# Kernel optimization log

Measured on AMD Instinct MI355X. Metric: run time of the kernel, lower is better.

The kernel has to match this reference:

```python
import jax, jax.numpy as jnp
import numpy as np

N_NODES = 50000
N_EDGES = 800000
VOCAB = 1000
EMBED = 64
HIDDEN = 64
N_CLASSES = 10
N_GRAPHS = 512


def setup_inputs() -> dict:
    key = jax.random.key(0)
    ks = jax.random.split(key, 10)
    tokens = jax.random.randint(ks[0], (N_NODES,), 0, VOCAB)
    edge_index = jax.random.randint(ks[1], (2, N_EDGES), 0, N_NODES)
    batch = jnp.sort(jax.random.randint(ks[2], (N_NODES,), 0, N_GRAPHS))
    emb = jax.random.normal(ks[3], (VOCAB, EMBED), jnp.float32) * 0.02
    emb = emb.at[0].set(0.0)  # padding_idx=0
    W1 = jax.random.normal(ks[4], (EMBED, HIDDEN), jnp.float32) * (1.0 / np.sqrt(EMBED))
    b1 = jnp.zeros((HIDDEN,), jnp.float32)
    W2 = jax.random.normal(ks[5], (HIDDEN, HIDDEN), jnp.float32) * (1.0 / np.sqrt(HIDDEN))
    b2 = jnp.zeros((HIDDEN,), jnp.float32)
    lin_W = jax.random.normal(ks[6], (HIDDEN, N_CLASSES), jnp.float32) * (1.0 / np.sqrt(HIDDEN))
    lin_b = jnp.zeros((N_CLASSES,), jnp.float32)
    return {"tokens": tokens, "edge_index": edge_index, "batch": batch,
            "emb": emb, "W1": W1, "b1": b1, "W2": W2, "b2": b2,
            "lin_W": lin_W, "lin_b": lin_b}


def _gcn_conv(x, src, dst, W, b, n_nodes):
    # PyG GCNConv: add self-loops, symmetric normalization D^-1/2 (A+I) D^-1/2
    ones = jnp.ones((src.shape[0],), x.dtype)
    deg = jax.ops.segment_sum(ones, dst, num_segments=n_nodes) + 1.0  # self-loop
    dis = jnp.where(deg > 0, jax.lax.rsqrt(deg), 0.0)
    h = x @ W  # linear first (no bias)
    coef = dis[src] * dis[dst]                      # [E]
    msg = h[src] * coef[:, None]                    # gather + scale
    agg = jax.ops.segment_sum(msg, dst, num_segments=n_nodes)
    agg = agg + h * (dis * dis)[:, None]            # self-loop message
    return agg + b


def reference(tokens, edge_index, batch, emb, W1, b1, W2, b2, lin_W, lin_b):
    src, dst = edge_index[0], edge_index[1]
    x = emb[tokens]                                  # [N, EMBED]
    x = jax.nn.relu(_gcn_conv(x, src, dst, W1, b1, N_NODES))
    x = jax.nn.relu(_gcn_conv(x, src, dst, W2, b2, N_NODES))
    # global_mean_pool over batch ids
    sums = jax.ops.segment_sum(x, batch, num_segments=N_GRAPHS)
    cnts = jax.ops.segment_sum(jnp.ones((x.shape[0],), x.dtype), batch, num_segments=N_GRAPHS)
    pooled = sums / jnp.maximum(cnts, 1.0)[:, None]  # [G, HIDDEN]
    return pooled @ lin_W + lin_b
```

## Files before the change

### kernel.cpp

```cpp
#include <hip/hip_runtime.h>

#define NGRAPHS 512
#define D 64
#define NCLS 10
#define MAXDEG 64
#define MDSH 6

__global__ void k_deg(const int* __restrict__ dst, int* __restrict__ degi,
                      int* __restrict__ rank, int E) {
  int i = blockIdx.x * blockDim.x + threadIdx.x;
  if (i < E) rank[i] = atomicAdd(&degi[dst[i]], 1);
}

__global__ __launch_bounds__(256) void k_fused2(
    const int* __restrict__ src, const int* __restrict__ dst,
    const int* __restrict__ rank, const int* __restrict__ tokens,
    int2* __restrict__ ec2, int E,
    const int* __restrict__ degi, float* __restrict__ dis, int n,
    const float* __restrict__ emb, const float* __restrict__ W1,
    float4* __restrict__ ht4, int ntok, int fillBlocks, int disBlocks,
    int tokBlocks) {
  if (blockIdx.x < fillBlocks) {
    int e = blockIdx.x * 256 + threadIdx.x;
    if (e < E) {
      int s = src[e];
      int rk = rank[e];
      if (rk < MAXDEG)
        ec2[((size_t)dst[e] << MDSH) + rk] = make_int2(s, tokens[s]);
    }
    return;
  }
  if (blockIdx.x < fillBlocks + disBlocks) {
    int i = (blockIdx.x - fillBlocks) * 256 + threadIdx.x;
    if (i < n) dis[i] = rsqrtf((float)degi[i] + 1.0f);
    return;
  }
  __shared__ float Ws[64 * 64];
  int tid = threadIdx.x;
  for (int i = tid; i < 64 * 64; i += 256) Ws[i] = W1[i];
  __syncthreads();
  const float4* Ws4 = (const float4*)Ws;
  int w = tid >> 6, lane = tid & 63;
  int cg = lane & 15;
  int kb = lane & 48;
  int bid = blockIdx.x - fillBlocks - disBlocks;
  for (int tok = bid * 4 + w; tok < ntok; tok += tokBlocks * 4) {
    float xval = emb[(size_t)tok * D + lane];
    float4 acc = make_float4(0.f, 0.f, 0.f, 0.f);
#pragma unroll
    for (int p = 0; p < 16; ++p) {
      float xv = __shfl(xval, kb + p, 64);
      float4 wv = Ws4[(kb + p) * 16 + cg];
      acc.x += xv * wv.x; acc.y += xv * wv.y;
      acc.z += xv * wv.z; acc.w += xv * wv.w;
    }
    acc.x += __shfl_xor(acc.x, 16, 64); acc.y += __shfl_xor(acc.y, 16, 64);
    acc.z += __shfl_xor(acc.z, 16, 64); acc.w += __shfl_xor(acc.w, 16, 64);
    acc.x += __shfl_xor(acc.x, 32, 64); acc.y += __shfl_xor(acc.y, 32, 64);
    acc.z += __shfl_xor(acc.z, 32, 64); acc.w += __shfl_xor(acc.w, 32, 64);
    if (lane < 16) ht4[(size_t)tok * 16 + cg] = acc;
  }
}

__global__ __launch_bounds__(256) void k_agg1t(const float4* __restrict__ ht4,
                                               const int2* __restrict__ ec2,
                                               const int* __restrict__ degi,
                                               const int* __restrict__ tokens,
                                               const float* __restrict__ dis,
                                               const float4* __restrict__ b14,
                                               float4* __restrict__ out, int n) {
  int tid = blockIdx.x * blockDim.x + threadIdx.x;
  int node = tid >> 6;
  int lane = tid & 63;
  int slot = lane >> 4;
  int cg = lane & 15;
  if (node >= n) return;
  int beg = node << MDSH;
  int end = beg + min(degi[node], MAXDEG);
  float4 acc = make_float4(0.f, 0.f, 0.f, 0.f);
  int j = beg + slot;
  for (; j + 12 < end; j += 16) {
    int2 e0 = ec2[j], e1 = ec2[j + 4], e2 = ec2[j + 8], e3 = ec2[j + 12];
    float w0 = dis[e0.x], w1 = dis[e1.x], w2 = dis[e2.x], w3 = dis[e3.x];
    float4 v0 = ht4[(size_t)e0.y * 16 + cg];
    float4 v1 = ht4[(size_t)e1.y * 16 + cg];
    float4 v2 = ht4[(size_t)e2.y * 16 + cg];
    float4 v3 = ht4[(size_t)e3.y * 16 + cg];
    acc.x += w0 * v0.x + w1 * v1.x + w2 * v2.x + w3 * v3.x;
    acc.y += w0 * v0.y + w1 * v1.y + w2 * v2.y + w3 * v3.y;
    acc.z += w0 * v0.z + w1 * v1.z + w2 * v2.z + w3 * v3.z;
    acc.w += w0 * v0.w + w1 * v1.w + w2 * v2.w + w3 * v3.w;
  }
  for (; j < end; j += 4) {
    int2 e = ec2[j];
    float w = dis[e.x];
    float4 v = ht4[(size_t)e.y * 16 + cg];
    acc.x += w * v.x; acc.y += w * v.y; acc.z += w * v.z; acc.w += w * v.w;
  }
  acc.x += __shfl_xor(acc.x, 16, 64); acc.y += __shfl_xor(acc.y, 16, 64);
  acc.z += __shfl_xor(acc.z, 16, 64); acc.w += __shfl_xor(acc.w, 16, 64);
  acc.x += __shfl_xor(acc.x, 32, 64); acc.y += __shfl_xor(acc.y, 32, 64);
  acc.z += __shfl_xor(acc.z, 32, 64); acc.w += __shfl_xor(acc.w, 32, 64);
  if (slot == 0) {
    float dd = dis[node];
    float4 vd = ht4[(size_t)tokens[node] * 16 + cg];
    float4 bv = b14[cg];
    float4 r;
    r.x = dd * fmaxf(dd * (acc.x + dd * vd.x) + bv.x, 0.f);
    r.y = dd * fmaxf(dd * (acc.y + dd * vd.y) + bv.y, 0.f);
    r.z = dd * fmaxf(dd * (acc.z + dd * vd.z) + bv.z, 0.f);
    r.w = dd * fmaxf(dd * (acc.w + dd * vd.w) + bv.w, 0.f);
    out[(size_t)node * 16 + cg] = r;
  }
}

__global__ __launch_bounds__(256) void k_gemmp(const float* __restrict__ x,
                                               const float* __restrict__ W,
                                               float4* __restrict__ o4, int n) {
  __shared__ float Ws[64 * 64];
  int tid = threadIdx.x;
  for (int i = tid; i < 64 * 64; i += 256) Ws[i] = W[i];
  __syncthreads();
  const float4* Ws4 = (const float4*)Ws;
  int w = tid >> 6, lane = tid & 63;
  int cg = lane & 15;
  int kb = lane & 48;
  for (int node = blockIdx.x * 4 + w; node < n; node += gridDim.x * 4) {
    float xval = x[(size_t)node * D + lane];
    float4 acc = make_float4(0.f, 0.f, 0.f, 0.f);
#pragma unroll
    for (int p = 0; p < 16; ++p) {
      float xv = __shfl(xval, kb + p, 64);
      float4 wv = Ws4[(kb + p) * 16 + cg];
      acc.x += xv * wv.x; acc.y += xv * wv.y;
      acc.z += xv * wv.z; acc.w += xv * wv.w;
    }
    acc.x += __shfl_xor(acc.x, 16, 64); acc.y += __shfl_xor(acc.y, 16, 64);
    acc.z += __shfl_xor(acc.z, 16, 64); acc.w += __shfl_xor(acc.w, 16, 64);
    acc.x += __shfl_xor(acc.x, 32, 64); acc.y += __shfl_xor(acc.y, 32, 64);
    acc.z += __shfl_xor(acc.z, 32, 64); acc.w += __shfl_xor(acc.w, 32, 64);
    if (lane < 16) o4[(size_t)node * 16 + cg] = acc;
  }
}

__global__ __launch_bounds__(256) void k_aggs(const float4* __restrict__ h4,
                                              const int2* __restrict__ ec2,
                                              const int* __restrict__ degi,
                                              const float* __restrict__ dis,
                                              const float4* __restrict__ b24,
                                              float4* __restrict__ out, int n) {
  int tid = blockIdx.x * blockDim.x + threadIdx.x;
  int node = tid >> 6;
  int lane = tid & 63;
  int slot = lane >> 4;
  int cg = lane & 15;
  if (node >= n) return;
  int beg = node << MDSH;
  int end = beg + min(degi[node], MAXDEG);
  float4 acc = make_float4(0.f, 0.f, 0.f, 0.f);
  int i = beg + slot;
  for (; i + 12 < end; i += 16) {
    int s0 = ec2[i].x, s1 = ec2[i + 4].x, s2 = ec2[i + 8].x, s3 = ec2[i + 12].x;
    float4 v0 = h4[(size_t)s0 * 16 + cg];
    float4 v1 = h4[(size_t)s1 * 16 + cg];
    float4 v2 = h4[(size_t)s2 * 16 + cg];
    float4 v3 = h4[(size_t)s3 * 16 + cg];
    acc.x += (v0.x + v1.x) + (v2.x + v3.x);
    acc.y += (v0.y + v1.y) + (v2.y + v3.y);
    acc.z += (v0.z + v1.z) + (v2.z + v3.z);
    acc.w += (v0.w + v1.w) + (v2.w + v3.w);
  }
  for (; i < end; i += 4) {
    float4 v = h4[(size_t)ec2[i].x * 16 + cg];
    acc.x += v.x; acc.y += v.y; acc.z += v.z; acc.w += v.w;
  }
  acc.x += __shfl_xor(acc.x, 16, 64); acc.y += __shfl_xor(acc.y, 16, 64);
  acc.z += __shfl_xor(acc.z, 16, 64); acc.w += __shfl_xor(acc.w, 16, 64);
  acc.x += __shfl_xor(acc.x, 32, 64); acc.y += __shfl_xor(acc.y, 32, 64);
  acc.z += __shfl_xor(acc.z, 32, 64); acc.w += __shfl_xor(acc.w, 32, 64);
  if (slot == 0) {
    float dd = dis[node];
    float4 hv = h4[(size_t)node * 16 + cg];
    float4 bv = b24[cg];
    acc.x = fmaxf(dd * (acc.x + hv.x) + bv.x, 0.f);
    acc.y = fmaxf(dd * (acc.y + hv.y) + bv.y, 0.f);
    acc.z = fmaxf(dd * (acc.z + hv.z) + bv.z, 0.f);
    acc.w = fmaxf(dd * (acc.w + hv.w) + bv.w, 0.f);
    out[(size_t)node * 16 + cg] = acc;
  }
}

__device__ __forceinline__ int lower_bound(const int* __restrict__ a, int n, int v) {
  int lo = 0, hi = n;
  while (lo < hi) {
    int m = (lo + hi) >> 1;
    if (a[m] < v) lo = m + 1; else hi = m;
  }
  return lo;
}

__global__ __launch_bounds__(256) void k_poolfinal(const float* __restrict__ x,
                                                   const int* __restrict__ batch,
                                                   const float* __restrict__ lw,
                                                   const float* __restrict__ lb,
                                                   float* __restrict__ out, int n) {
  __shared__ float red[4][64];
  __shared__ float pooled[64];
  int g = blockIdx.x;
  int s = lower_bound(batch, n, g);
  int e = lower_bound(batch, n, g + 1);
  int w = threadIdx.x >> 6, lane = threadIdx.x & 63;
  float acc = 0.f;
  for (int i = s + w; i < e; i += 4) acc += x[(size_t)i * D + lane];
  red[w][lane] = acc;
  __syncthreads();
  if (w == 0) {
    float v = red[0][lane] + red[1][lane] + red[2][lane] + red[3][lane];
    pooled[lane] = v / fmaxf((float)(e - s), 1.0f);
  }
  __syncthreads();
  if (threadIdx.x < NCLS) {
    int c = threadIdx.x;
    float a = lb[c];
#pragma unroll
    for (int k = 0; k < D; ++k) a += pooled[k] * lw[k * NCLS + c];
    out[g * NCLS + c] = a;
  }
}

extern "C" void kernel_launch(void* const* d_in, const int* in_sizes, int n_in,
                              void* d_out, int out_size, void* d_ws, size_t ws_size,
                              hipStream_t stream) {
  const int* tokens = (const int*)d_in[0];
  const int* edge   = (const int*)d_in[1];
  const int* batch  = (const int*)d_in[2];
  const float* emb  = (const float*)d_in[3];
  const float* W1   = (const float*)d_in[4];
  const float* b1   = (const float*)d_in[5];
  const float* W2   = (const float*)d_in[6];
  const float* b2   = (const float*)d_in[7];
  const float* lw   = (const float*)d_in[8];
  const float* lb   = (const float*)d_in[9];
  float* out = (float*)d_out;

  const int N = in_sizes[0];
  const int E = in_sizes[1] / 2;
  const int ntok = in_sizes[3] / D;
  const int* src  = edge;
  const int* dstv = edge + E;

  char* ws = (char*)d_ws;
  size_t off = 0;
  auto alloc = [&](size_t bytes) {
    void* p = ws + off;
    off += (bytes + 255) & ~(size_t)255;
    return p;
  };
  float* A    = (float*)alloc((size_t)N * D * sizeof(float));
  float* B    = (float*)alloc((size_t)N * D * sizeof(float));
  int2*  ec2  = (int2*)alloc((size_t)N * MAXDEG * sizeof(int2));
  int*   rank = (int*)alloc((size_t)E * sizeof(int));
  float* dis  = (float*)alloc((size_t)N * sizeof(float));
  int*   degi = (int*)alloc((size_t)N * sizeof(int));
  float* ht   = (float*)alloc((size_t)ntok * D * sizeof(float));

  hipMemsetAsync(degi, 0, (size_t)N * sizeof(int), stream);

  k_deg<<<(E + 255) / 256, 256, 0, stream>>>(dstv, degi, rank, E);

  const int fillBlocks = (E + 255) / 256;
  const int disBlocks = (N + 255) / 256;
  const int tokBlocks = (ntok + 3) / 4;
  k_fused2<<<fillBlocks + disBlocks + tokBlocks, 256, 0, stream>>>(
      src, dstv, rank, tokens, ec2, E, degi, dis, N, emb, W1, (float4*)ht, ntok,
      fillBlocks, disBlocks, tokBlocks);

  const int nodeBlocks = (N + 3) / 4;
  const int gemmGrid = 2048;

  k_agg1t<<<nodeBlocks, 256, 0, stream>>>((const float4*)ht, ec2, degi, tokens,
                                          dis, (const float4*)b1, (float4*)B, N);
  k_gemmp<<<gemmGrid, 256, 0, stream>>>(B, W2, (float4*)A, N);
  k_aggs<<<nodeBlocks, 256, 0, stream>>>((const float4*)A, ec2, degi, dis,
                                         (const float4*)b2, (float4*)B, N);
  k_poolfinal<<<NGRAPHS, 256, 0, stream>>>(B, batch, lw, lb, out, N);
}
```

Baseline: 157.5 us.

## Fuse layer-1 aggregation with W2 GEMM and pooling into layer-2 aggregation

Merges the layer-1 aggregation kernel with the following 64x64 GEMM, so each wave aggregates a node and immediately multiplies the result by W2 held in shared memory. This drops the intermediate B buffer round trip. It also fuses mean-pool accumulation into the layer-2 aggregation through float atomics into per-graph sums. A small final kernel computes the classifier output, and the degi memset is extended to zero the sums buffer. The atomics add contention on 512 graph rows and make the summation order nondeterministic.

```diff
diff --git a/kernel.cpp b/kernel.cpp
--- a/kernel.cpp
+++ b/kernel.cpp
@@ -62,93 +62,89 @@
   }
 }
 
-__global__ __launch_bounds__(256) void k_agg1t(const float4* __restrict__ ht4,
+__global__ __launch_bounds__(256) void k_agg1g(const float4* __restrict__ ht4,
                                                const int2* __restrict__ ec2,
                                                const int* __restrict__ degi,
                                                const int* __restrict__ tokens,
                                                const float* __restrict__ dis,
                                                const float4* __restrict__ b14,
-                                               float4* __restrict__ out, int n) {
-  int tid = blockIdx.x * blockDim.x + threadIdx.x;
-  int node = tid >> 6;
-  int lane = tid & 63;
-  int slot = lane >> 4;
-  int cg = lane & 15;
-  if (node >= n) return;
-  int beg = node << MDSH;
-  int end = beg + min(degi[node], MAXDEG);
-  float4 acc = make_float4(0.f, 0.f, 0.f, 0.f);
-  int j = beg + slot;
-  for (; j + 12 < end; j += 16) {
-    int2 e0 = ec2[j], e1 = ec2[j + 4], e2 = ec2[j + 8], e3 = ec2[j + 12];
-    float w0 = dis[e0.x], w1 = dis[e1.x], w2 = dis[e2.x], w3 = dis[e3.x];
-    float4 v0 = ht4[(size_t)e0.y * 16 + cg];
-    float4 v1 = ht4[(size_t)e1.y * 16 + cg];
-    float4 v2 = ht4[(size_t)e2.y * 16 + cg];
-    float4 v3 = ht4[(size_t)e3.y * 16 + cg];
-    acc.x += w0 * v0.x + w1 * v1.x + w2 * v2.x + w3 * v3.x;
-    acc.y += w0 * v0.y + w1 * v1.y + w2 * v2.y + w3 * v3.y;
-    acc.z += w0 * v0.z + w1 * v1.z + w2 * v2.z + w3 * v3.z;
-    acc.w += w0 * v0.w + w1 * v1.w + w2 * v2.w + w3 * v3.w;
-  }
-  for (; j < end; j += 4) {
-    int2 e = ec2[j];
-    float w = dis[e.x];
-    float4 v = ht4[(size_t)e.y * 16 + cg];
-    acc.x += w * v.x; acc.y += w * v.y; acc.z += w * v.z; acc.w += w * v.w;
-  }
-  acc.x += __shfl_xor(acc.x, 16, 64); acc.y += __shfl_xor(acc.y, 16, 64);
-  acc.z += __shfl_xor(acc.z, 16, 64); acc.w += __shfl_xor(acc.w, 16, 64);
-  acc.x += __shfl_xor(acc.x, 32, 64); acc.y += __shfl_xor(acc.y, 32, 64);
-  acc.z += __shfl_xor(acc.z, 32, 64); acc.w += __shfl_xor(acc.w, 32, 64);
-  if (slot == 0) {
-    float dd = dis[node];
-    float4 vd = ht4[(size_t)tokens[node] * 16 + cg];
-    float4 bv = b14[cg];
-    float4 r;
-    r.x = dd * fmaxf(dd * (acc.x + dd * vd.x) + bv.x, 0.f);
-    r.y = dd * fmaxf(dd * (acc.y + dd * vd.y) + bv.y, 0.f);
-    r.z = dd * fmaxf(dd * (acc.z + dd * vd.z) + bv.z, 0.f);
-    r.w = dd * fmaxf(dd * (acc.w + dd * vd.w) + bv.w, 0.f);
-    out[(size_t)node * 16 + cg] = r;
-  }
-}
-
-__global__ __launch_bounds__(256) void k_gemmp(const float* __restrict__ x,
-                                               const float* __restrict__ W,
-                                               float4* __restrict__ o4, int n) {
+                                               const float* __restrict__ W2,
+                                               float4* __restrict__ h2, int n) {
   __shared__ float Ws[64 * 64];
   int tid = threadIdx.x;
-  for (int i = tid; i < 64 * 64; i += 256) Ws[i] = W[i];
+  for (int i = tid; i < 64 * 64; i += 256) Ws[i] = W2[i];
   __syncthreads();
   const float4* Ws4 = (const float4*)Ws;
   int w = tid >> 6, lane = tid & 63;
-  int cg = lane & 15;
+  int slot = lane >> 4, cg = lane & 15;
   int kb = lane & 48;
   for (int node = blockIdx.x * 4 + w; node < n; node += gridDim.x * 4) {
-    float xval = x[(size_t)node * D + lane];
+    int beg = node << MDSH;
+    int end = beg + min(degi[node], MAXDEG);
     float4 acc = make_float4(0.f, 0.f, 0.f, 0.f);
-#pragma unroll
-    for (int p = 0; p < 16; ++p) {
-      float xv = __shfl(xval, kb + p, 64);
-      float4 wv = Ws4[(kb + p) * 16 + cg];
-      acc.x += xv * wv.x; acc.y += xv * wv.y;
-      acc.z += xv * wv.z; acc.w += xv * wv.w;
+    int j = beg + slot;
+    for (; j + 12 < end; j += 16) {
+      int2 e0 = ec2[j], e1 = ec2[j + 4], e2 = ec2[j + 8], e3 = ec2[j + 12];
+      float w0 = dis[e0.x], w1 = dis[e1.x], w2 = dis[e2.x], w3 = dis[e3.x];
+      float4 v0 = ht4[(size_t)e0.y * 16 + cg];
+      float4 v1 = ht4[(size_t)e1.y * 16 + cg];
+      float4 v2 = ht4[(size_t)e2.y * 16 + cg];
+      float4 v3 = ht4[(size_t)e3.y * 16 + cg];
+      acc.x += w0 * v0.x + w1 * v1.x + w2 * v2.x + w3 * v3.x;
+      acc.y += w0 * v0.y + w1 * v1.y + w2 * v2.y + w3 * v3.y;
+      acc.z += w0 * v0.z + w1 * v1.z + w2 * v2.z + w3 * v3.z;
+      acc.w += w0 * v0.w + w1 * v1.w + w2 * v2.w + w3 * v3.w;
+    }
+    for (; j < end; j += 4) {
+      int2 e = ec2[j];
+      float wq = dis[e.x];
+      float4 v = ht4[(size_t)e.y * 16 + cg];
+      acc.x += wq * v.x; acc.y += wq * v.y; acc.z += wq * v.z; acc.w += wq * v.w;
     }
     acc.x += __shfl_xor(acc.x, 16, 64); acc.y += __shfl_xor(acc.y, 16, 64);
     acc.z += __shfl_xor(acc.z, 16, 64); acc.w += __shfl_xor(acc.w, 16, 64);
     acc.x += __shfl_xor(acc.x, 32, 64); acc.y += __shfl_xor(acc.y, 32, 64);
     acc.z += __shfl_xor(acc.z, 32, 64); acc.w += __shfl_xor(acc.w, 32, 64);
-    if (lane < 16) o4[(size_t)node * 16 + cg] = acc;
-  }
-}
-
-__global__ __launch_bounds__(256) void k_aggs(const float4* __restrict__ h4,
+    float dd = dis[node];
+    float4 vd = ht4[(size_t)tokens[node] * 16 + cg];
+    float4 bv = b14[cg];
+    float4 x2;
+    x2.x = dd * fmaxf(dd * (acc.x + dd * vd.x) + bv.x, 0.f);
+    x2.y = dd * fmaxf(dd * (acc.y + dd * vd.y) + bv.y, 0.f);
+    x2.z = dd * fmaxf(dd * (acc.z + dd * vd.z) + bv.z, 0.f);
+    x2.w = dd * fmaxf(dd * (acc.w + dd * vd.w) + bv.w, 0.f);
+    float4 g = make_float4(0.f, 0.f, 0.f, 0.f);
+#pragma unroll
+    for (int p = 0; p < 4; ++p) {
+      int sl = (kb >> 2) + p;
+      float xv0 = __shfl(x2.x, sl, 64);
+      float xv1 = __shfl(x2.y, sl, 64);
+      float xv2 = __shfl(x2.z, sl, 64);
+      float xv3 = __shfl(x2.w, sl, 64);
+      float4 w0 = Ws4[(kb + 4 * p + 0) * 16 + cg];
+      float4 w1 = Ws4[(kb + 4 * p + 1) * 16 + cg];
+      float4 w2 = Ws4[(kb + 4 * p + 2) * 16 + cg];
+      float4 w3 = Ws4[(kb + 4 * p + 3) * 16 + cg];
+      g.x += xv0 * w0.x + xv1 * w1.x + xv2 * w2.x + xv3 * w3.x;
+      g.y += xv0 * w0.y + xv1 * w1.y + xv2 * w2.y + xv3 * w3.y;
+      g.z += xv0 * w0.z + xv1 * w1.z + xv2 * w2.z + xv3 * w3.z;
+      g.w += xv0 * w0.w + xv1 * w1.w + xv2 * w2.w + xv3 * w3.w;
+    }
+    g.x += __shfl_xor(g.x, 16, 64); g.y += __shfl_xor(g.y, 16, 64);
+    g.z += __shfl_xor(g.z, 16, 64); g.w += __shfl_xor(g.w, 16, 64);
+    g.x += __shfl_xor(g.x, 32, 64); g.y += __shfl_xor(g.y, 32, 64);
+    g.z += __shfl_xor(g.z, 32, 64); g.w += __shfl_xor(g.w, 32, 64);
+    if (lane < 16) h2[(size_t)node * 16 + cg] = g;
+  }
+}
+
+__global__ __launch_bounds__(256) void k_aggp(const float4* __restrict__ h4,
                                               const int2* __restrict__ ec2,
                                               const int* __restrict__ degi,
                                               const float* __restrict__ dis,
                                               const float4* __restrict__ b24,
-                                              float4* __restrict__ out, int n) {
+                                              const int* __restrict__ batch,
+                                              float* __restrict__ sums, int n) {
   int tid = blockIdx.x * blockDim.x + threadIdx.x;
   int node = tid >> 6;
   int lane = tid & 63;
@@ -182,11 +178,14 @@
     float dd = dis[node];
     float4 hv = h4[(size_t)node * 16 + cg];
     float4 bv = b24[cg];
-    acc.x = fmaxf(dd * (acc.x + hv.x) + bv.x, 0.f);
-    acc.y = fmaxf(dd * (acc.y + hv.y) + bv.y, 0.f);
-    acc.z = fmaxf(dd * (acc.z + hv.z) + bv.z, 0.f);
-    acc.w = fmaxf(dd * (acc.w + hv.w) + bv.w, 0.f);
-    out[(size_t)node * 16 + cg] = acc;
+    float4 r;
+    r.x = fmaxf(dd * (acc.x + hv.x) + bv.x, 0.f);
+    r.y = fmaxf(dd * (acc.y + hv.y) + bv.y, 0.f);
+    r.z = fmaxf(dd * (acc.z + hv.z) + bv.z, 0.f);
+    r.w = fmaxf(dd * (acc.w + hv.w) + bv.w, 0.f);
+    float* sp = sums + (size_t)batch[node] * 64 + cg * 4;
+    atomicAdd(sp + 0, r.x); atomicAdd(sp + 1, r.y);
+    atomicAdd(sp + 2, r.z); atomicAdd(sp + 3, r.w);
   }
 }
 
@@ -199,33 +198,19 @@
   return lo;
 }
 
-__global__ __launch_bounds__(256) void k_poolfinal(const float* __restrict__ x,
-                                                   const int* __restrict__ batch,
-                                                   const float* __restrict__ lw,
-                                                   const float* __restrict__ lb,
-                                                   float* __restrict__ out, int n) {
-  __shared__ float red[4][64];
-  __shared__ float pooled[64];
-  int g = blockIdx.x;
+__global__ void k_final(const float* __restrict__ sums, const int* __restrict__ batch,
+                        const float* __restrict__ lw, const float* __restrict__ lb,
+                        float* __restrict__ out, int n) {
+  int i = blockIdx.x * blockDim.x + threadIdx.x;
+  if (i >= NGRAPHS * NCLS) return;
+  int g = i / NCLS, c = i - g * NCLS;
   int s = lower_bound(batch, n, g);
   int e = lower_bound(batch, n, g + 1);
-  int w = threadIdx.x >> 6, lane = threadIdx.x & 63;
-  float acc = 0.f;
-  for (int i = s + w; i < e; i += 4) acc += x[(size_t)i * D + lane];
-  red[w][lane] = acc;
-  __syncthreads();
-  if (w == 0) {
-    float v = red[0][lane] + red[1][lane] + red[2][lane] + red[3][lane];
-    pooled[lane] = v / fmaxf((float)(e - s), 1.0f);
-  }
-  __syncthreads();
-  if (threadIdx.x < NCLS) {
-    int c = threadIdx.x;
-    float a = lb[c];
+  float inv = 1.0f / fmaxf((float)(e - s), 1.0f);
+  float a = lb[c];
 #pragma unroll
-    for (int k = 0; k < D; ++k) a += pooled[k] * lw[k * NCLS + c];
-    out[g * NCLS + c] = a;
-  }
+  for (int k = 0; k < D; ++k) a += sums[g * 64 + k] * inv * lw[k * NCLS + c];
+  out[i] = a;
 }
 
 extern "C" void kernel_launch(void* const* d_in, const int* in_sizes, int n_in,
@@ -257,14 +242,15 @@
     return p;
   };
   float* A    = (float*)alloc((size_t)N * D * sizeof(float));
-  float* B    = (float*)alloc((size_t)N * D * sizeof(float));
   int2*  ec2  = (int2*)alloc((size_t)N * MAXDEG * sizeof(int2));
   int*   rank = (int*)alloc((size_t)E * sizeof(int));
   float* dis  = (float*)alloc((size_t)N * sizeof(float));
   int*   degi = (int*)alloc((size_t)N * sizeof(int));
+  float* sums = (float*)alloc((size_t)NGRAPHS * D * sizeof(float));
   float* ht   = (float*)alloc((size_t)ntok * D * sizeof(float));
 
-  hipMemsetAsync(degi, 0, (size_t)N * sizeof(int), stream);
+  size_t zbytes = (size_t)(((char*)sums + (size_t)NGRAPHS * D * sizeof(float)) - (char*)degi);
+  hipMemsetAsync(degi, 0, zbytes, stream);
 
   k_deg<<<(E + 255) / 256, 256, 0, stream>>>(dstv, degi, rank, E);
 
@@ -275,13 +261,12 @@
       src, dstv, rank, tokens, ec2, E, degi, dis, N, emb, W1, (float4*)ht, ntok,
       fillBlocks, disBlocks, tokBlocks);
 
+  k_agg1g<<<2048, 256, 0, stream>>>((const float4*)ht, ec2, degi, tokens, dis,
+                                    (const float4*)b1, W2, (float4*)A, N);
+
   const int nodeBlocks = (N + 3) / 4;
-  const int gemmGrid = 2048;
-
-  k_agg1t<<<nodeBlocks, 256, 0, stream>>>((const float4*)ht, ec2, degi, tokens,
-                                          dis, (const float4*)b1, (float4*)B, N);
-  k_gemmp<<<gemmGrid, 256, 0, stream>>>(B, W2, (float4*)A, N);
-  k_aggs<<<nodeBlocks, 256, 0, stream>>>((const float4*)A, ec2, degi, dis,
-                                         (const float4*)b2, (float4*)B, N);
-  k_poolfinal<<<NGRAPHS, 256, 0, stream>>>(B, batch, lw, lb, out, N);
-}
+  k_aggp<<<nodeBlocks, 256, 0, stream>>>((const float4*)A, ec2, degi, dis,
+                                         (const float4*)b2, batch, sums, N);
+
+  k_final<<<(NGRAPHS * NCLS + 255) / 256, 256, 0, stream>>>(sums, batch, lw, lb, out, N);
+}
```

New measurement: 192.5 us. +22.2%, slower.

## Reorder layer-2 as aggregate-then-transform and fuse W2 GEMM into pooling

Applied to the files above, without the earlier changes.

Layer 2 now aggregates the pre-scaled layer-1 output first, then applies W2, using the linearity (A·X)·W = A·(X·W). The separate per-node GEMM kernel is removed. The W2 multiply, bias, ReLU and mean-pool are fused into one per-graph kernel, which drops a full N×64 write and read plus one launch. In exchange, the pooling stage now runs only 512 blocks that each do the GEMM for their graph's nodes, which could underuse the GPU and adds per-block work.

```diff
diff --git a/kernel.cpp b/kernel.cpp
--- a/kernel.cpp
+++ b/kernel.cpp
@@ -82,10 +82,10 @@
   for (; j + 12 < end; j += 16) {
     int2 e0 = ec2[j], e1 = ec2[j + 4], e2 = ec2[j + 8], e3 = ec2[j + 12];
     float w0 = dis[e0.x], w1 = dis[e1.x], w2 = dis[e2.x], w3 = dis[e3.x];
-    float4 v0 = ht4[(size_t)e0.y * 16 + cg];
-    float4 v1 = ht4[(size_t)e1.y * 16 + cg];
-    float4 v2 = ht4[(size_t)e2.y * 16 + cg];
-    float4 v3 = ht4[(size_t)e3.y * 16 + cg];
+    float4 v0 = ht4[((size_t)e0.y << 4) + cg];
+    float4 v1 = ht4[((size_t)e1.y << 4) + cg];
+    float4 v2 = ht4[((size_t)e2.y << 4) + cg];
+    float4 v3 = ht4[((size_t)e3.y << 4) + cg];
     acc.x += w0 * v0.x + w1 * v1.x + w2 * v2.x + w3 * v3.x;
     acc.y += w0 * v0.y + w1 * v1.y + w2 * v2.y + w3 * v3.y;
     acc.z += w0 * v0.z + w1 * v1.z + w2 * v2.z + w3 * v3.z;
@@ -94,7 +94,7 @@
   for (; j < end; j += 4) {
     int2 e = ec2[j];
     float w = dis[e.x];
-    float4 v = ht4[(size_t)e.y * 16 + cg];
+    float4 v = ht4[((size_t)e.y << 4) + cg];
     acc.x += w * v.x; acc.y += w * v.y; acc.z += w * v.z; acc.w += w * v.w;
   }
   acc.x += __shfl_xor(acc.x, 16, 64); acc.y += __shfl_xor(acc.y, 16, 64);
@@ -103,30 +103,91 @@
   acc.z += __shfl_xor(acc.z, 32, 64); acc.w += __shfl_xor(acc.w, 32, 64);
   if (slot == 0) {
     float dd = dis[node];
-    float4 vd = ht4[(size_t)tokens[node] * 16 + cg];
+    float4 vd = ht4[((size_t)tokens[node] << 4) + cg];
     float4 bv = b14[cg];
     float4 r;
     r.x = dd * fmaxf(dd * (acc.x + dd * vd.x) + bv.x, 0.f);
     r.y = dd * fmaxf(dd * (acc.y + dd * vd.y) + bv.y, 0.f);
     r.z = dd * fmaxf(dd * (acc.z + dd * vd.z) + bv.z, 0.f);
     r.w = dd * fmaxf(dd * (acc.w + dd * vd.w) + bv.w, 0.f);
-    out[(size_t)node * 16 + cg] = r;
-  }
-}
-
-__global__ __launch_bounds__(256) void k_gemmp(const float* __restrict__ x,
-                                               const float* __restrict__ W,
-                                               float4* __restrict__ o4, int n) {
+    out[((size_t)node << 4) + cg] = r;
+  }
+}
+
+__global__ __launch_bounds__(256) void k_aggz(const float4* __restrict__ h4,
+                                              const int2* __restrict__ ec2,
+                                              const int* __restrict__ degi,
+                                              float4* __restrict__ out, int n) {
+  int tid = blockIdx.x * blockDim.x + threadIdx.x;
+  int node = tid >> 6;
+  int lane = tid & 63;
+  int slot = lane >> 4;
+  int cg = lane & 15;
+  if (node >= n) return;
+  int beg = node << MDSH;
+  int end = beg + min(degi[node], MAXDEG);
+  float4 acc = make_float4(0.f, 0.f, 0.f, 0.f);
+  int i = beg + slot;
+  for (; i + 12 < end; i += 16) {
+    int s0 = ec2[i].x, s1 = ec2[i + 4].x, s2 = ec2[i + 8].x, s3 = ec2[i + 12].x;
+    float4 v0 = h4[((size_t)s0 << 4) + cg];
+    float4 v1 = h4[((size_t)s1 << 4) + cg];
+    float4 v2 = h4[((size_t)s2 << 4) + cg];
+    float4 v3 = h4[((size_t)s3 << 4) + cg];
+    acc.x += (v0.x + v1.x) + (v2.x + v3.x);
+    acc.y += (v0.y + v1.y) + (v2.y + v3.y);
+    acc.z += (v0.z + v1.z) + (v2.z + v3.z);
+    acc.w += (v0.w + v1.w) + (v2.w + v3.w);
+  }
+  for (; i < end; i += 4) {
+    float4 v = h4[((size_t)ec2[i].x << 4) + cg];
+    acc.x += v.x; acc.y += v.y; acc.z += v.z; acc.w += v.w;
+  }
+  acc.x += __shfl_xor(acc.x, 16, 64); acc.y += __shfl_xor(acc.y, 16, 64);
+  acc.z += __shfl_xor(acc.z, 16, 64); acc.w += __shfl_xor(acc.w, 16, 64);
+  acc.x += __shfl_xor(acc.x, 32, 64); acc.y += __shfl_xor(acc.y, 32, 64);
+  acc.z += __shfl_xor(acc.z, 32, 64); acc.w += __shfl_xor(acc.w, 32, 64);
+  if (slot == 0) {
+    float4 hv = h4[((size_t)node << 4) + cg];
+    acc.x += hv.x; acc.y += hv.y; acc.z += hv.z; acc.w += hv.w;
+    out[((size_t)node << 4) + cg] = acc;
+  }
+}
+
+__device__ __forceinline__ int lower_bound(const int* __restrict__ a, int n, int v) {
+  int lo = 0, hi = n;
+  while (lo < hi) {
+    int m = (lo + hi) >> 1;
+    if (a[m] < v) lo = m + 1; else hi = m;
+  }
+  return lo;
+}
+
+__global__ __launch_bounds__(256) void k_poolgemm(const float* __restrict__ z,
+                                                  const int* __restrict__ batch,
+                                                  const float* __restrict__ dis,
+                                                  const float* __restrict__ W2,
+                                                  const float* __restrict__ b2,
+                                                  const float* __restrict__ lw,
+                                                  const float* __restrict__ lb,
+                                                  float* __restrict__ out, int n) {
   __shared__ float Ws[64 * 64];
+  __shared__ float4 red4[4][16];
+  __shared__ float pooled[64];
   int tid = threadIdx.x;
-  for (int i = tid; i < 64 * 64; i += 256) Ws[i] = W[i];
+  for (int i = tid; i < 64 * 64; i += 256) Ws[i] = W2[i];
   __syncthreads();
   const float4* Ws4 = (const float4*)Ws;
+  int g = blockIdx.x;
+  int s = lower_bound(batch, n, g);
+  int e = lower_bound(batch, n, g + 1);
   int w = tid >> 6, lane = tid & 63;
   int cg = lane & 15;
   int kb = lane & 48;
-  for (int node = blockIdx.x * 4 + w; node < n; node += gridDim.x * 4) {
-    float xval = x[(size_t)node * D + lane];
+  float4 pacc = make_float4(0.f, 0.f, 0.f, 0.f);
+  float4 bv = ((const float4*)b2)[cg];
+  for (int node = s + w; node < e; node += 4) {
+    float xval = z[(size_t)node * D + lane];
     float4 acc = make_float4(0.f, 0.f, 0.f, 0.f);
 #pragma unroll
     for (int p = 0; p < 16; ++p) {
@@ -139,88 +200,25 @@
     acc.z += __shfl_xor(acc.z, 16, 64); acc.w += __shfl_xor(acc.w, 16, 64);
     acc.x += __shfl_xor(acc.x, 32, 64); acc.y += __shfl_xor(acc.y, 32, 64);
     acc.z += __shfl_xor(acc.z, 32, 64); acc.w += __shfl_xor(acc.w, 32, 64);
-    if (lane < 16) o4[(size_t)node * 16 + cg] = acc;
-  }
-}
-
-__global__ __launch_bounds__(256) void k_aggs(const float4* __restrict__ h4,
-                                              const int2* __restrict__ ec2,
-                                              const int* __restrict__ degi,
-                                              const float* __restrict__ dis,
-                                              const float4* __restrict__ b24,
-                                              float4* __restrict__ out, int n) {
-  int tid = blockIdx.x * blockDim.x + threadIdx.x;
-  int node = tid >> 6;
-  int lane = tid & 63;
-  int slot = lane >> 4;
-  int cg = lane & 15;
-  if (node >= n) return;
-  int beg = node << MDSH;
-  int end = beg + min(degi[node], MAXDEG);
-  float4 acc = make_float4(0.f, 0.f, 0.f, 0.f);
-  int i = beg + slot;
-  for (; i + 12 < end; i += 16) {
-    int s0 = ec2[i].x, s1 = ec2[i + 4].x, s2 = ec2[i + 8].x, s3 = ec2[i + 12].x;
-    float4 v0 = h4[(size_t)s0 * 16 + cg];
-    float4 v1 = h4[(size_t)s1 * 16 + cg];
-    float4 v2 = h4[(size_t)s2 * 16 + cg];
-    float4 v3 = h4[(size_t)s3 * 16 + cg];
-    acc.x += (v0.x + v1.x) + (v2.x + v3.x);
-    acc.y += (v0.y + v1.y) + (v2.y + v3.y);
-    acc.z += (v0.z + v1.z) + (v2.z + v3.z);
-    acc.w += (v0.w + v1.w) + (v2.w + v3.w);
-  }
-  for (; i < end; i += 4) {
-    float4 v = h4[(size_t)ec2[i].x * 16 + cg];
-    acc.x += v.x; acc.y += v.y; acc.z += v.z; acc.w += v.w;
-  }
-  acc.x += __shfl_xor(acc.x, 16, 64); acc.y += __shfl_xor(acc.y, 16, 64);
-  acc.z += __shfl_xor(acc.z, 16, 64); acc.w += __shfl_xor(acc.w, 16, 64);
-  acc.x += __shfl_xor(acc.x, 32, 64); acc.y += __shfl_xor(acc.y, 32, 64);
-  acc.z += __shfl_xor(acc.z, 32, 64); acc.w += __shfl_xor(acc.w, 32, 64);
-  if (slot == 0) {
     float dd = dis[node];
-    float4 hv = h4[(size_t)node * 16 + cg];
-    float4 bv = b24[cg];
-    acc.x = fmaxf(dd * (acc.x + hv.x) + bv.x, 0.f);
-    acc.y = fmaxf(dd * (acc.y + hv.y) + bv.y, 0.f);
-    acc.z = fmaxf(dd * (acc.z + hv.z) + bv.z, 0.f);
-    acc.w = fmaxf(dd * (acc.w + hv.w) + bv.w, 0.f);
-    out[(size_t)node * 16 + cg] = acc;
-  }
-}
-
-__device__ __forceinline__ int lower_bound(const int* __restrict__ a, int n, int v) {
-  int lo = 0, hi = n;
-  while (lo < hi) {
-    int m = (lo + hi) >> 1;
-    if (a[m] < v) lo = m + 1; else hi = m;
-  }
-  return lo;
-}
-
-__global__ __launch_bounds__(256) void k_poolfinal(const float* __restrict__ x,
-                                                   const int* __restrict__ batch,
-                                                   const float* __restrict__ lw,
-                                                   const float* __restrict__ lb,
-                                                   float* __restrict__ out, int n) {
-  __shared__ float red[4][64];
-  __shared__ float pooled[64];
-  int g = blockIdx.x;
-  int s = lower_bound(batch, n, g);
-  int e = lower_bound(batch, n, g + 1);
-  int w = threadIdx.x >> 6, lane = threadIdx.x & 63;
-  float acc = 0.f;
-  for (int i = s + w; i < e; i += 4) acc += x[(size_t)i * D + lane];
-  red[w][lane] = acc;
-  __syncthreads();
-  if (w == 0) {
-    float v = red[0][lane] + red[1][lane] + red[2][lane] + red[3][lane];
-    pooled[lane] = v / fmaxf((float)(e - s), 1.0f);
-  }
-  __syncthreads();
-  if (threadIdx.x < NCLS) {
-    int c = threadIdx.x;
+    pacc.x += fmaxf(dd * acc.x + bv.x, 0.f);
+    pacc.y += fmaxf(dd * acc.y + bv.y, 0.f);
+    pacc.z += fmaxf(dd * acc.z + bv.z, 0.f);
+    pacc.w += fmaxf(dd * acc.w + bv.w, 0.f);
+  }
+  if ((lane >> 4) == 0) red4[w][cg] = pacc;
+  __syncthreads();
+  if (tid < 64) {
+    const float* r0 = (const float*)&red4[0][0];
+    const float* r1 = (const float*)&red4[1][0];
+    const float* r2 = (const float*)&red4[2][0];
+    const float* r3 = (const float*)&red4[3][0];
+    float v = r0[tid] + r1[tid] + r2[tid] + r3[tid];
+    pooled[tid] = v / fmaxf((float)(e - s), 1.0f);
+  }
+  __syncthreads();
+  if (tid < NCLS) {
+    int c = tid;
     float a = lb[c];
 #pragma unroll
     for (int k = 0; k < D; ++k) a += pooled[k] * lw[k * NCLS + c];
@@ -276,12 +274,11 @@
       fillBlocks, disBlocks, tokBlocks);
 
   const int nodeBlocks = (N + 3) / 4;
-  const int gemmGrid = 2048;
 
   k_agg1t<<<nodeBlocks, 256, 0, stream>>>((const float4*)ht, ec2, degi, tokens,
                                           dis, (const float4*)b1, (float4*)B, N);
-  k_gemmp<<<gemmGrid, 256, 0, stream>>>(B, W2, (float4*)A, N);
-  k_aggs<<<nodeBlocks, 256, 0, stream>>>((const float4*)A, ec2, degi, dis,
-                                         (const float4*)b2, (float4*)B, N);
-  k_poolfinal<<<NGRAPHS, 256, 0, stream>>>(B, batch, lw, lb, out, N);
-}
+
+  k_aggz<<<nodeBlocks, 256, 0, stream>>>((const float4*)B, ec2, degi, (float4*)A, N);
+
+  k_poolgemm<<<NGRAPHS, 256, 0, stream>>>(A, batch, dis, W2, b2, lw, lb, out, N);
+}
```

New measurement: 161.7 us. +2.7%, slower.
